# Performance work log

Hardware: AMD Instinct MI355X
Metric: run time of the kernel (lower is better)

The kernel has to match this reference:

```python
import jax, jax.numpy as jnp
import numpy as np


def _conv1x1(x, w, b):
    # x: [B, C, N], w: [O, C], b: [O]  (Conv1d with kernel_size=1)
    return jnp.einsum('bcn,oc->bon', x, w) + b[None, :, None]


def setup_inputs() -> dict:
    key = jax.random.key(0)
    ks = jax.random.split(key, 16)
    B, N, OD, A, H, M = 4096, 64, 128, 16, 64, 32
    s = jnp.float32(0.05)
    inp = {}
    inp['obs'] = jax.random.normal(ks[0], (B, OD, N), jnp.float32)
    inp['actions'] = jax.random.normal(ks[1], (N, B, A), jnp.float32)
    inp['relations'] = jax.random.uniform(ks[2], (N, B, N - 1), jnp.float32)
    # ObsEncode stand-in: 2-layer 1x1-conv MLP obs_dim -> 64 -> 64
    inp['enc_w1'] = jax.random.normal(ks[3], (H, OD), jnp.float32) * s
    inp['enc_b1'] = jnp.zeros((H,), jnp.float32)
    inp['enc_w2'] = jax.random.normal(ks[4], (H, H), jnp.float32) * s
    inp['enc_b2'] = jnp.zeros((H,), jnp.float32)
    C = H + A  # hidden_dim + act_dim = 80
    inp['cv_w1'] = jax.random.normal(ks[5], (M, C), jnp.float32) * s
    inp['cv_b1'] = jnp.zeros((M,), jnp.float32)
    inp['cv_w2'] = jax.random.normal(ks[6], (M // 2, M), jnp.float32) * s
    inp['cv_b2'] = jnp.zeros((M // 2,), jnp.float32)
    inp['sv_w1'] = jax.random.normal(ks[7], (M, C), jnp.float32) * s
    inp['sv_b1'] = jnp.zeros((M,), jnp.float32)
    inp['sv_w2'] = jax.random.normal(ks[8], (M // 2, M), jnp.float32) * s
    inp['sv_b2'] = jnp.zeros((M // 2,), jnp.float32)
    inp['pf_w'] = jax.random.normal(ks[9], (A, M), jnp.float32) * s
    inp['pf_b'] = jnp.zeros((A,), jnp.float32)
    inp['task'] = 0
    inp['agent_divide'] = N
    return inp


def reference(obs, actions, relations, enc_w1, enc_b1, enc_w2, enc_b2,
              cv_w1, cv_b1, cv_w2, cv_b2, sv_w1, sv_b1, sv_w2, sv_b2,
              pf_w, pf_b, task, agent_divide):
    N = relations.shape[0]
    # ObsEncode (use_relation=False): task/relations unused
    h = jax.nn.relu(_conv1x1(obs, enc_w1, enc_b1))
    h = _conv1x1(h, enc_w2, enc_b2)  # [B, 64, N]
    act = jnp.transpose(actions, (1, 2, 0))  # [B, A, N]
    sa = jnp.concatenate([h, act], axis=1)  # [B, 80, N]
    role1 = sa[:, :, :agent_divide]  # agent_divide == N -> full
    cv = _conv1x1(jax.nn.relu(_conv1x1(role1, cv_w1, cv_b1)), cv_w2, cv_b2)  # [B,16,N]
    sv = _conv1x1(jax.nn.relu(_conv1x1(role1, sv_w1, sv_b1)), sv_w2, sv_b2)  # [B,16,N]
    # build rel: insert self-weight 1 at column n_a for each agent (vectorized)
    n = jnp.arange(N)[:, None]  # agent index
    j = jnp.arange(N)[None, :]  # output column
    src = jnp.clip(jnp.where(j < n, j, j - 1), 0, N - 2)  # [N, N]
    g = jnp.take_along_axis(relations, src[:, None, :], axis=2)  # [N, B, N]
    rel = jnp.where((j == n)[:, None, :], jnp.float32(1.0), g)  # [N, B, N]
    rel = jnp.transpose(rel, (1, 2, 0))  # [B, N(cols j), N(agents)]
    cv = jnp.einsum('bcj,bjn->bcn', cv, rel)  # [B, 16, N]
    cat = jnp.concatenate([cv, sv], axis=1)  # [B, 32, N]
    post = _conv1x1(cat, pf_w, pf_b)  # [B, A, N]
    post = jnp.transpose(post, (2, 0, 1))  # [N, B, A]
    action_taken = jnp.argmax(actions, axis=2)[..., None]  # [N, B, 1]
    q = jnp.take_along_axis(post, action_taken, axis=2)  # [N, B, 1]
    return q
```

## Files before the change

kernel.cpp:

```cpp
#include <hip/hip_runtime.h>

namespace {
constexpr int Bb = 4096;
constexpr int Nn = 64;
constexpr int OD = 128;

constexpr int REL_OFF  = 0;
constexpr int CVV_OFF  = 4160;
constexpr int SVV_OFF  = 5184;
constexpr int PART_OFF = 6208;
}

typedef __attribute__((ext_vector_type(8))) _Float16 f16x8;
typedef __attribute__((ext_vector_type(4))) float    f32x4;

__device__ __forceinline__ void splitAs(const float* wrow, int k0, f16x8& ph, f16x8& pl) {
  float4 f0 = *(const float4*)(wrow + k0);
  float4 f1 = *(const float4*)(wrow + k0 + 4);
  float v[8] = {f0.x, f0.y, f0.z, f0.w, f1.x, f1.y, f1.z, f1.w};
#pragma unroll
  for (int i = 0; i < 8; ++i) {
    _Float16 h = (_Float16)v[i];
    ph[i] = h;
    pl[i] = (_Float16)((v[i] - (float)h) * 1024.f);
  }
}

__device__ __forceinline__ void loadBs(const float* X, int n, int k0,
                                       f16x8& bh, f16x8& bl) {
#pragma unroll
  for (int i = 0; i < 8; ++i) {
    float v = X[(k0 + i) * Nn + n];
    _Float16 h = (_Float16)v;
    bh[i] = h;
    bl[i] = (_Float16)((v - (float)h) * 1024.f);
  }
}

__global__ __launch_bounds__(256, 2)
void critic_fused(const float* __restrict__ obs,
                  const float* __restrict__ actions,
                  const float* __restrict__ relations,
                  const float* __restrict__ enc_w1, const float* __restrict__ enc_b1,
                  const float* __restrict__ enc_w2, const float* __restrict__ enc_b2,
                  const float* __restrict__ cv_w1, const float* __restrict__ cv_b1,
                  const float* __restrict__ cv_w2, const float* __restrict__ cv_b2,
                  const float* __restrict__ sv_w1, const float* __restrict__ sv_b1,
                  const float* __restrict__ sv_w2, const float* __restrict__ sv_b2,
                  const float* __restrict__ pf_w, const float* __restrict__ pf_b,
                  float* __restrict__ out)
{
  __shared__ float buf0[8192];
  __shared__ float buf1[4096];
  __shared__ float sa_s[96 * 64];
  __shared__ int   amax_s[64];

  const int tid = threadIdx.x;
  const int b = blockIdx.x;
  const int lane = tid & 63;
  const int w = tid >> 6;
  const int lo16 = lane & 15;
  const int hig  = lane >> 4;
  const int o0 = w * 16;

  {
    const float4* src = (const float4*)(obs + (size_t)b * OD * Nn);
    float4* dst = (float4*)buf0;
#pragma unroll
    for (int i = 0; i < 8; ++i) dst[tid + i * 256] = src[tid + i * 256];
  }
  for (int idx = tid; idx < Nn * 16; idx += 256) {
    int n = idx >> 4, a = idx & 15;
    sa_s[(64 + a) * Nn + n] = actions[((size_t)n * Bb + b) * 16 + a];
  }
  {
    float4* z = (float4*)(sa_s + 80 * Nn);
    z[tid] = make_float4(0.f, 0.f, 0.f, 0.f);
  }
  __syncthreads();

  {
    const float* wr = enc_w1 + (size_t)(o0 + lo16) * OD;
    f32x4 hac[4] = {};
    f32x4 lac[4] = {};
#pragma unroll
    for (int kk = 0; kk < 4; ++kk) {
      int k0 = kk * 32 + hig * 8;
      f16x8 ah, al;
      splitAs(wr, k0, ah, al);
#pragma unroll
      for (int t = 0; t < 4; ++t) {
        f16x8 bh, bl;
        loadBs(buf0, t * 16 + lo16, k0, bh, bl);
        hac[t] = __builtin_amdgcn_mfma_f32_16x16x32_f16(ah, bh, hac[t], 0, 0, 0);
        lac[t] = __builtin_amdgcn_mfma_f32_16x16x32_f16(ah, bl, lac[t], 0, 0, 0);
        lac[t] = __builtin_amdgcn_mfma_f32_16x16x32_f16(al, bh, lac[t], 0, 0, 0);
      }
    }
#pragma unroll
    for (int t = 0; t < 4; ++t)
#pragma unroll
      for (int r = 0; r < 4; ++r) {
        int o = o0 + hig * 4 + r;
        float v = hac[t][r] + lac[t][r] * (1.f / 1024.f) + enc_b1[o];
        buf1[o * Nn + t * 16 + lo16] = fmaxf(v, 0.f);
      }
  }
  __syncthreads();

  for (int idx = tid; idx < 4096; idx += 256) {
    int n = idx >> 6, k = idx & 63;
    if (k < 63) {
      float v = relations[((size_t)n * Bb + b) * 63 + k];
      int j = (k < n) ? k : k + 1;
      buf0[REL_OFF + n * 65 + j] = v;
    } else {
      buf0[REL_OFF + n * 65 + n] = 1.0f;
    }
  }
  if (tid < Nn) {
    float best = sa_s[64 * Nn + tid]; int bi = 0;
#pragma unroll
    for (int a = 1; a < 16; ++a) {
      float v = sa_s[(64 + a) * Nn + tid];
      if (v > best) { best = v; bi = a; }
    }
    amax_s[tid] = bi;
  }
  {
    const float* wr = enc_w2 + (size_t)(o0 + lo16) * 64;
    f32x4 hac[4] = {};
    f32x4 lac[4] = {};
#pragma unroll
    for (int kk = 0; kk < 2; ++kk) {
      int k0 = kk * 32 + hig * 8;
      f16x8 ah, al;
      splitAs(wr, k0, ah, al);
#pragma unroll
      for (int t = 0; t < 4; ++t) {
        f16x8 bh, bl;
        loadBs(buf1, t * 16 + lo16, k0, bh, bl);
        hac[t] = __builtin_amdgcn_mfma_f32_16x16x32_f16(ah, bh, hac[t], 0, 0, 0);
        lac[t] = __builtin_amdgcn_mfma_f32_16x16x32_f16(ah, bl, lac[t], 0, 0, 0);
        lac[t] = __builtin_amdgcn_mfma_f32_16x16x32_f16(al, bh, lac[t], 0, 0, 0);
      }
    }
#pragma unroll
    for (int t = 0; t < 4; ++t)
#pragma unroll
      for (int r = 0; r < 4; ++r) {
        int o = o0 + hig * 4 + r;
        sa_s[o * Nn + t * 16 + lo16] = hac[t][r] + lac[t][r] * (1.f / 1024.f) + enc_b2[o];
      }
  }
  __syncthreads();

  {
    int row = o0 + lo16;
    const float* wr = (row < 32) ? (cv_w1 + (size_t)row * 80)
                                 : (sv_w1 + (size_t)(row - 32) * 80);
    f32x4 hac[4] = {};
    f32x4 lac[4] = {};
#pragma unroll
    for (int kk = 0; kk < 3; ++kk) {
      int k0 = kk * 32 + hig * 8;
      f16x8 ah = {}, al = {};
      if (k0 < 80) splitAs(wr, k0, ah, al);
#pragma unroll
      for (int t = 0; t < 4; ++t) {
        f16x8 bh, bl;
        loadBs(sa_s, t * 16 + lo16, k0, bh, bl);
        hac[t] = __builtin_amdgcn_mfma_f32_16x16x32_f16(ah, bh, hac[t], 0, 0, 0);
        lac[t] = __builtin_amdgcn_mfma_f32_16x16x32_f16(ah, bl, lac[t], 0, 0, 0);
        lac[t] = __builtin_amdgcn_mfma_f32_16x16x32_f16(al, bh, lac[t], 0, 0, 0);
      }
    }
#pragma unroll
    for (int t = 0; t < 4; ++t)
#pragma unroll
      for (int r = 0; r < 4; ++r) {
        int o = o0 + hig * 4 + r;
        float bb = (o < 32) ? cv_b1[o] : sv_b1[o - 32];
        float v = hac[t][r] + lac[t][r] * (1.f / 1024.f) + bb;
        buf1[o * Nn + t * 16 + lo16] = fmaxf(v, 0.f);
      }
  }
  __syncthreads();

  {
    const int p4n0 = (tid & 31) * 2;
    const int p4o0 = (tid >> 5) * 4;
    const float* wr[4]; float bb[4];
    int srow; float* dst; int dro;
    if (p4o0 < 16) {
      srow = 0; dst = buf0 + CVV_OFF; dro = p4o0;
#pragma unroll
      for (int i = 0; i < 4; ++i) { wr[i] = cv_w2 + (p4o0 + i) * 32; bb[i] = cv_b2[p4o0 + i]; }
    } else {
      srow = 32; dst = buf0 + SVV_OFF; dro = p4o0 - 16;
#pragma unroll
      for (int i = 0; i < 4; ++i) { wr[i] = sv_w2 + (p4o0 + i - 16) * 32; bb[i] = sv_b2[p4o0 + i - 16]; }
    }
    float acc[4][2];
#pragma unroll
    for (int i = 0; i < 4; ++i) { acc[i][0] = bb[i]; acc[i][1] = bb[i]; }
#pragma unroll 2
    for (int c = 0; c < 32; c += 4) {
      float wv[4][4];
#pragma unroll
      for (int i = 0; i < 4; ++i) {
        float4 t = *(const float4*)(wr[i] + c);
        wv[i][0]=t.x; wv[i][1]=t.y; wv[i][2]=t.z; wv[i][3]=t.w;
      }
#pragma unroll
      for (int k = 0; k < 4; ++k) {
        float2 ov = *(const float2*)(buf1 + (srow + c + k) * Nn + p4n0);
#pragma unroll
        for (int i = 0; i < 4; ++i) {
          acc[i][0] = fmaf(wv[i][k], ov.x, acc[i][0]);
          acc[i][1] = fmaf(wv[i][k], ov.y, acc[i][1]);
        }
      }
    }
#pragma unroll
    for (int i = 0; i < 4; ++i)
      *(float2*)(dst + (dro + i) * Nn + p4n0) = make_float2(acc[i][0], acc[i][1]);
  }
  __syncthreads();

  {
    const int n = tid & 63, cg = tid >> 6;
    const float* cvv = buf0 + CVV_OFF;
    const float* svv = buf0 + SVV_OFF;
    const float* rel = buf0 + REL_OFF + n * 65;
    float acc[4] = {0.f, 0.f, 0.f, 0.f};
#pragma unroll 4
    for (int j = 0; j < 64; j += 4) {
      float r0 = rel[j], r1 = rel[j+1], r2 = rel[j+2], r3 = rel[j+3];
#pragma unroll
      for (int c4 = 0; c4 < 4; ++c4) {
        float4 cv = *(const float4*)(cvv + (cg * 4 + c4) * Nn + j);
        acc[c4] = fmaf(cv.x, r0, acc[c4]);
        acc[c4] = fmaf(cv.y, r1, acc[c4]);
        acc[c4] = fmaf(cv.z, r2, acc[c4]);
        acc[c4] = fmaf(cv.w, r3, acc[c4]);
      }
    }
    int a = amax_s[n];
    const float* pw = pf_w + a * 32;
    float part = 0.f;
#pragma unroll
    for (int c4 = 0; c4 < 4; ++c4) {
      part = fmaf(acc[c4], pw[cg * 4 + c4], part);
      part = fmaf(svv[(cg * 4 + c4) * Nn + n], pw[16 + cg * 4 + c4], part);
    }
    buf0[PART_OFF + cg * 64 + n] = part;
  }
  __syncthreads();

  if (tid < Nn) {
    float q = pf_b[amax_s[tid]]
            + buf0[PART_OFF + tid]       + buf0[PART_OFF + 64 + tid]
            + buf0[PART_OFF + 128 + tid] + buf0[PART_OFF + 192 + tid];
    out[(size_t)tid * Bb + b] = q;
  }
}

extern "C" void kernel_launch(void* const* d_in, const int* in_sizes, int n_in,
                              void* d_out, int out_size, void* d_ws, size_t ws_size,
                              hipStream_t stream) {
  const float* obs       = (const float*)d_in[0];
  const float* actions   = (const float*)d_in[1];
  const float* relations = (const float*)d_in[2];
  const float* enc_w1    = (const float*)d_in[3];
  const float* enc_b1    = (const float*)d_in[4];
  const float* enc_w2    = (const float*)d_in[5];
  const float* enc_b2    = (const float*)d_in[6];
  const float* cv_w1     = (const float*)d_in[7];
  const float* cv_b1     = (const float*)d_in[8];
  const float* cv_w2     = (const float*)d_in[9];
  const float* cv_b2     = (const float*)d_in[10];
  const float* sv_w1     = (const float*)d_in[11];
  const float* sv_b1     = (const float*)d_in[12];
  const float* sv_w2     = (const float*)d_in[13];
  const float* sv_b2     = (const float*)d_in[14];
  const float* pf_w      = (const float*)d_in[15];
  const float* pf_b      = (const float*)d_in[16];

  critic_fused<<<dim3(Bb), dim3(256), 0, stream>>>(
      obs, actions, relations,
      enc_w1, enc_b1, enc_w2, enc_b2,
      cv_w1, cv_b1, cv_w2, cv_b2,
      sv_w1, sv_b1, sv_w2, sv_b2,
      pf_w, pf_b, (float*)d_out);
}
```

Measured before the change: 159.0 us.

## Pre-split weights into fp16 fragments and stage swizzled fp16 activations in LDS

A small pre-kernel converts the MFMA weights once per call into hi/lo fp16 pairs laid out in per-lane fragment order in the workspace. The main kernel then loads each weight fragment with one vector load instead of splitting it per block. Activations are converted to hi/lo fp16 once when written to shared memory, using an XOR-swizzled n-major layout, so B operands are read as 16-byte vectors instead of eight strided scalar reads with repeated conversion. It adds an extra kernel launch and a workspace dependency, and reorganises shared memory, which changes LDS usage and may affect occupancy.

```diff
diff --git a/kernel.cpp b/kernel.cpp
--- a/kernel.cpp
+++ b/kernel.cpp
@@ -5,55 +5,87 @@
 constexpr int Nn = 64;
 constexpr int OD = 128;
 
-constexpr int REL_OFF  = 0;
-constexpr int CVV_OFF  = 4160;
-constexpr int SVV_OFF  = 5184;
-constexpr int PART_OFF = 6208;
+constexpr int E1H = 0;
+constexpr int E1L = 8192;
+constexpr int E2H = 16384;
+constexpr int E2L = 20480;
+constexpr int C1H = 24576;
+constexpr int C1L = 30720;
+constexpr int WS_ELEMS = 36864;
 }
 
 typedef __attribute__((ext_vector_type(8))) _Float16 f16x8;
+typedef __attribute__((ext_vector_type(4))) _Float16 f16x4;
 typedef __attribute__((ext_vector_type(4))) float    f32x4;
 
-__device__ __forceinline__ void splitAs(const float* wrow, int k0, f16x8& ph, f16x8& pl) {
-  float4 f0 = *(const float4*)(wrow + k0);
-  float4 f1 = *(const float4*)(wrow + k0 + 4);
-  float v[8] = {f0.x, f0.y, f0.z, f0.w, f1.x, f1.y, f1.z, f1.w};
-#pragma unroll
-  for (int i = 0; i < 8; ++i) {
-    _Float16 h = (_Float16)v[i];
-    ph[i] = h;
-    pl[i] = (_Float16)((v[i] - (float)h) * 1024.f);
-  }
-}
-
-__device__ __forceinline__ void loadBs(const float* X, int n, int k0,
-                                       f16x8& bh, f16x8& bl) {
-#pragma unroll
-  for (int i = 0; i < 8; ++i) {
-    float v = X[(k0 + i) * Nn + n];
-    _Float16 h = (_Float16)v;
-    bh[i] = h;
-    bl[i] = (_Float16)((v - (float)h) * 1024.f);
-  }
+__device__ __forceinline__ int swz(int n, int rowb, int k) {
+  return n * rowb + ((2 * k) ^ ((n & 7) << 4));
+}
+__device__ __forceinline__ int swz4(int n, int rowb, int k) {
+  return n * rowb + ((2 * k) ^ ((n & 3) << 4));
+}
+
+__global__ __launch_bounds__(256)
+void prep_weights(const float* __restrict__ ew1, const float* __restrict__ ew2,
+                  const float* __restrict__ cw1, const float* __restrict__ sw1,
+                  _Float16* __restrict__ ws) {
+  int idx = blockIdx.x * 256 + threadIdx.x;
+  if (idx >= 18432) return;
+  int pos, hbase, lbase;
+  float v;
+  if (idx < 8192) {
+    pos = idx; hbase = E1H; lbase = E1L;
+    int frag = pos >> 9, r = pos & 511, lane = r >> 3, i = r & 7;
+    int w = frag >> 2, kk = frag & 3;
+    int row = w * 16 + (lane & 15), k = kk * 32 + (lane >> 4) * 8 + i;
+    v = ew1[row * 128 + k];
+  } else if (idx < 12288) {
+    pos = idx - 8192; hbase = E2H; lbase = E2L;
+    int frag = pos >> 9, r = pos & 511, lane = r >> 3, i = r & 7;
+    int w = frag >> 1, kk = frag & 1;
+    int row = w * 16 + (lane & 15), k = kk * 32 + (lane >> 4) * 8 + i;
+    v = ew2[row * 64 + k];
+  } else {
+    pos = idx - 12288; hbase = C1H; lbase = C1L;
+    int frag = pos >> 9, r = pos & 511, lane = r >> 3, i = r & 7;
+    int w = frag / 3, kk = frag % 3;
+    int row = w * 16 + (lane & 15), k = kk * 32 + (lane >> 4) * 8 + i;
+    v = 0.f;
+    if (k < 80) v = (row < 32) ? cw1[row * 80 + k] : sw1[(row - 32) * 80 + k];
+  }
+  _Float16 h = (_Float16)v;
+  ws[hbase + pos] = h;
+  ws[lbase + pos] = (_Float16)((v - (float)h) * 1024.f);
 }
 
 __global__ __launch_bounds__(256, 2)
 void critic_fused(const float* __restrict__ obs,
                   const float* __restrict__ actions,
                   const float* __restrict__ relations,
-                  const float* __restrict__ enc_w1, const float* __restrict__ enc_b1,
-                  const float* __restrict__ enc_w2, const float* __restrict__ enc_b2,
-                  const float* __restrict__ cv_w1, const float* __restrict__ cv_b1,
+                  const float* __restrict__ enc_b1, const float* __restrict__ enc_b2,
+                  const float* __restrict__ cv_b1,  const float* __restrict__ sv_b1,
                   const float* __restrict__ cv_w2, const float* __restrict__ cv_b2,
-                  const float* __restrict__ sv_w1, const float* __restrict__ sv_b1,
                   const float* __restrict__ sv_w2, const float* __restrict__ sv_b2,
                   const float* __restrict__ pf_w, const float* __restrict__ pf_b,
+                  const _Float16* __restrict__ ws,
                   float* __restrict__ out)
 {
-  __shared__ float buf0[8192];
-  __shared__ float buf1[4096];
-  __shared__ float sa_s[96 * 64];
-  __shared__ int   amax_s[64];
+  __shared__ float rel_s[64 * 65];
+  __shared__ __align__(16) char RA[32768];
+  __shared__ __align__(16) char RB[16384];
+  __shared__ __align__(16) char RC[8192];
+  __shared__ int amax_s[64];
+
+  char* X0h = RA;
+  char* X0l = RA + 16384;
+  char* sah = RA;
+  char* sal = RA + 8192;
+  float* X3 = (float*)(RA + 16384);
+  char* X1h = RB;
+  char* X1l = RB + 8192;
+  float* csv  = (float*)RB;
+  char* acth = RC;
+  char* actl = RC + 4096;
 
   const int tid = threadIdx.x;
   const int b = blockIdx.x;
@@ -62,49 +94,81 @@
   const int lo16 = lane & 15;
   const int hig  = lane >> 4;
   const int o0 = w * 16;
-
-  {
-    const float4* src = (const float4*)(obs + (size_t)b * OD * Nn);
-    float4* dst = (float4*)buf0;
-#pragma unroll
-    for (int i = 0; i < 8; ++i) dst[tid + i * 256] = src[tid + i * 256];
-  }
-  for (int idx = tid; idx < Nn * 16; idx += 256) {
-    int n = idx >> 4, a = idx & 15;
-    sa_s[(64 + a) * Nn + n] = actions[((size_t)n * Bb + b) * 16 + a];
-  }
-  {
-    float4* z = (float4*)(sa_s + 80 * Nn);
-    z[tid] = make_float4(0.f, 0.f, 0.f, 0.f);
-  }
-  __syncthreads();
-
-  {
-    const float* wr = enc_w1 + (size_t)(o0 + lo16) * OD;
-    f32x4 hac[4] = {};
-    f32x4 lac[4] = {};
+  const f16x8* wsv = (const f16x8*)ws;
+
+  {
+    int n = tid & 63, chunk = tid >> 6;
+    const float* p = obs + (size_t)b * (OD * Nn) + (size_t)chunk * 32 * Nn + n;
+#pragma unroll
+    for (int g = 0; g < 4; ++g) {
+      f16x8 uh, ul;
+#pragma unroll
+      for (int j = 0; j < 8; ++j) {
+        float v = p[(g * 8 + j) * Nn];
+        _Float16 h = (_Float16)v;
+        uh[j] = h;
+        ul[j] = (_Float16)((v - (float)h) * 1024.f);
+      }
+      int off = swz(n, 256, chunk * 32 + g * 8);
+      *(f16x8*)(X0h + off) = uh;
+      *(f16x8*)(X0l + off) = ul;
+    }
+  }
+  {
+    int n = tid >> 2, a0 = (tid & 3) * 4;
+    float4 v4 = *(const float4*)(actions + ((size_t)n * Bb + b) * 16 + a0);
+    float vv[4] = {v4.x, v4.y, v4.z, v4.w};
+    f16x4 uh, ul;
+#pragma unroll
+    for (int r = 0; r < 4; ++r) {
+      _Float16 h = (_Float16)vv[r];
+      uh[r] = h;
+      ul[r] = (_Float16)((vv[r] - (float)h) * 1024.f);
+    }
+    int offa = swz4(n, 64, a0);
+    *(f16x4*)(acth + offa) = uh;
+    *(f16x4*)(actl + offa) = ul;
+    f16x4 z = {};
+    int offz = swz4(n, 64, 16 + a0);
+    *(f16x4*)(acth + offz) = z;
+    *(f16x4*)(actl + offz) = z;
+  }
+  __syncthreads();
+
+  {
+    f32x4 hac[4] = {}, lac[4] = {};
 #pragma unroll
     for (int kk = 0; kk < 4; ++kk) {
+      int frag = w * 4 + kk;
+      f16x8 ah = wsv[(E1H >> 3) + frag * 64 + lane];
+      f16x8 al = wsv[(E1L >> 3) + frag * 64 + lane];
       int k0 = kk * 32 + hig * 8;
-      f16x8 ah, al;
-      splitAs(wr, k0, ah, al);
 #pragma unroll
       for (int t = 0; t < 4; ++t) {
-        f16x8 bh, bl;
-        loadBs(buf0, t * 16 + lo16, k0, bh, bl);
+        int off = swz(t * 16 + lo16, 256, k0);
+        f16x8 bh = *(const f16x8*)(X0h + off);
+        f16x8 bl = *(const f16x8*)(X0l + off);
         hac[t] = __builtin_amdgcn_mfma_f32_16x16x32_f16(ah, bh, hac[t], 0, 0, 0);
         lac[t] = __builtin_amdgcn_mfma_f32_16x16x32_f16(ah, bl, lac[t], 0, 0, 0);
         lac[t] = __builtin_amdgcn_mfma_f32_16x16x32_f16(al, bh, lac[t], 0, 0, 0);
       }
     }
 #pragma unroll
-    for (int t = 0; t < 4; ++t)
+    for (int t = 0; t < 4; ++t) {
+      f16x4 ph, pl;
 #pragma unroll
       for (int r = 0; r < 4; ++r) {
         int o = o0 + hig * 4 + r;
         float v = hac[t][r] + lac[t][r] * (1.f / 1024.f) + enc_b1[o];
-        buf1[o * Nn + t * 16 + lo16] = fmaxf(v, 0.f);
-      }
+        v = fmaxf(v, 0.f);
+        _Float16 h = (_Float16)v;
+        ph[r] = h;
+        pl[r] = (_Float16)((v - (float)h) * 1024.f);
+      }
+      int off = swz(t * 16 + lo16, 128, o0 + hig * 4);
+      *(f16x4*)(X1h + off) = ph;
+      *(f16x4*)(X1l + off) = pl;
+    }
   }
   __syncthreads();
 
@@ -113,63 +177,77 @@
     if (k < 63) {
       float v = relations[((size_t)n * Bb + b) * 63 + k];
       int j = (k < n) ? k : k + 1;
-      buf0[REL_OFF + n * 65 + j] = v;
+      rel_s[n * 65 + j] = v;
     } else {
-      buf0[REL_OFF + n * 65 + n] = 1.0f;
+      rel_s[n * 65 + n] = 1.0f;
     }
   }
   if (tid < Nn) {
-    float best = sa_s[64 * Nn + tid]; int bi = 0;
+    const float* ar = actions + ((size_t)tid * Bb + b) * 16;
+    float best = ar[0]; int bi = 0;
 #pragma unroll
     for (int a = 1; a < 16; ++a) {
-      float v = sa_s[(64 + a) * Nn + tid];
+      float v = ar[a];
       if (v > best) { best = v; bi = a; }
     }
     amax_s[tid] = bi;
   }
   {
-    const float* wr = enc_w2 + (size_t)(o0 + lo16) * 64;
-    f32x4 hac[4] = {};
-    f32x4 lac[4] = {};
+    f32x4 hac[4] = {}, lac[4] = {};
 #pragma unroll
     for (int kk = 0; kk < 2; ++kk) {
+      int frag = w * 2 + kk;
+      f16x8 ah = wsv[(E2H >> 3) + frag * 64 + lane];
+      f16x8 al = wsv[(E2L >> 3) + frag * 64 + lane];
       int k0 = kk * 32 + hig * 8;
-      f16x8 ah, al;
-      splitAs(wr, k0, ah, al);
 #pragma unroll
       for (int t = 0; t < 4; ++t) {
-        f16x8 bh, bl;
-        loadBs(buf1, t * 16 + lo16, k0, bh, bl);
+        int off = swz(t * 16 + lo16, 128, k0);
+        f16x8 bh = *(const f16x8*)(X1h + off);
+        f16x8 bl = *(const f16x8*)(X1l + off);
         hac[t] = __builtin_amdgcn_mfma_f32_16x16x32_f16(ah, bh, hac[t], 0, 0, 0);
         lac[t] = __builtin_amdgcn_mfma_f32_16x16x32_f16(ah, bl, lac[t], 0, 0, 0);
         lac[t] = __builtin_amdgcn_mfma_f32_16x16x32_f16(al, bh, lac[t], 0, 0, 0);
       }
     }
 #pragma unroll
-    for (int t = 0; t < 4; ++t)
+    for (int t = 0; t < 4; ++t) {
+      f16x4 ph, pl;
 #pragma unroll
       for (int r = 0; r < 4; ++r) {
         int o = o0 + hig * 4 + r;
-        sa_s[o * Nn + t * 16 + lo16] = hac[t][r] + lac[t][r] * (1.f / 1024.f) + enc_b2[o];
-      }
-  }
-  __syncthreads();
-
-  {
-    int row = o0 + lo16;
-    const float* wr = (row < 32) ? (cv_w1 + (size_t)row * 80)
-                                 : (sv_w1 + (size_t)(row - 32) * 80);
-    f32x4 hac[4] = {};
-    f32x4 lac[4] = {};
+        float v = hac[t][r] + lac[t][r] * (1.f / 1024.f) + enc_b2[o];
+        _Float16 h = (_Float16)v;
+        ph[r] = h;
+        pl[r] = (_Float16)((v - (float)h) * 1024.f);
+      }
+      int off = swz(t * 16 + lo16, 128, o0 + hig * 4);
+      *(f16x4*)(sah + off) = ph;
+      *(f16x4*)(sal + off) = pl;
+    }
+  }
+  __syncthreads();
+
+  {
+    f32x4 hac[4] = {}, lac[4] = {};
 #pragma unroll
     for (int kk = 0; kk < 3; ++kk) {
-      int k0 = kk * 32 + hig * 8;
-      f16x8 ah = {}, al = {};
-      if (k0 < 80) splitAs(wr, k0, ah, al);
+      int frag = w * 3 + kk;
+      f16x8 ah = wsv[(C1H >> 3) + frag * 64 + lane];
+      f16x8 al = wsv[(C1L >> 3) + frag * 64 + lane];
 #pragma unroll
       for (int t = 0; t < 4; ++t) {
+        int n = t * 16 + lo16;
         f16x8 bh, bl;
-        loadBs(sa_s, t * 16 + lo16, k0, bh, bl);
+        if (kk < 2) {
+          int off = swz(n, 128, kk * 32 + hig * 8);
+          bh = *(const f16x8*)(sah + off);
+          bl = *(const f16x8*)(sal + off);
+        } else {
+          int off = swz4(n, 64, hig * 8);
+          bh = *(const f16x8*)(acth + off);
+          bl = *(const f16x8*)(actl + off);
+        }
         hac[t] = __builtin_amdgcn_mfma_f32_16x16x32_f16(ah, bh, hac[t], 0, 0, 0);
         lac[t] = __builtin_amdgcn_mfma_f32_16x16x32_f16(ah, bl, lac[t], 0, 0, 0);
         lac[t] = __builtin_amdgcn_mfma_f32_16x16x32_f16(al, bh, lac[t], 0, 0, 0);
@@ -182,7 +260,7 @@
         int o = o0 + hig * 4 + r;
         float bb = (o < 32) ? cv_b1[o] : sv_b1[o - 32];
         float v = hac[t][r] + lac[t][r] * (1.f / 1024.f) + bb;
-        buf1[o * Nn + t * 16 + lo16] = fmaxf(v, 0.f);
+        X3[o * Nn + t * 16 + lo16] = fmaxf(v, 0.f);
       }
   }
   __syncthreads();
@@ -193,11 +271,11 @@
     const float* wr[4]; float bb[4];
     int srow; float* dst; int dro;
     if (p4o0 < 16) {
-      srow = 0; dst = buf0 + CVV_OFF; dro = p4o0;
+      srow = 0; dst = csv; dro = p4o0;
 #pragma unroll
       for (int i = 0; i < 4; ++i) { wr[i] = cv_w2 + (p4o0 + i) * 32; bb[i] = cv_b2[p4o0 + i]; }
     } else {
-      srow = 32; dst = buf0 + SVV_OFF; dro = p4o0 - 16;
+      srow = 32; dst = csv + 1024; dro = p4o0 - 16;
 #pragma unroll
       for (int i = 0; i < 4; ++i) { wr[i] = sv_w2 + (p4o0 + i - 16) * 32; bb[i] = sv_b2[p4o0 + i - 16]; }
     }
@@ -214,7 +292,7 @@
       }
 #pragma unroll
       for (int k = 0; k < 4; ++k) {
-        float2 ov = *(const float2*)(buf1 + (srow + c + k) * Nn + p4n0);
+        float2 ov = *(const float2*)(X3 + (srow + c + k) * Nn + p4n0);
 #pragma unroll
         for (int i = 0; i < 4; ++i) {
           acc[i][0] = fmaf(wv[i][k], ov.x, acc[i][0]);
@@ -230,13 +308,13 @@
 
   {
     const int n = tid & 63, cg = tid >> 6;
-    const float* cvv = buf0 + CVV_OFF;
-    const float* svv = buf0 + SVV_OFF;
-    const float* rel = buf0 + REL_OFF + n * 65;
+    const float* cvv = csv;
+    const float* svv = csv + 1024;
+    const float* relr = rel_s + n * 65;
     float acc[4] = {0.f, 0.f, 0.f, 0.f};
 #pragma unroll 4
     for (int j = 0; j < 64; j += 4) {
-      float r0 = rel[j], r1 = rel[j+1], r2 = rel[j+2], r3 = rel[j+3];
+      float r0 = relr[j], r1 = relr[j+1], r2 = relr[j+2], r3 = relr[j+3];
 #pragma unroll
       for (int c4 = 0; c4 < 4; ++c4) {
         float4 cv = *(const float4*)(cvv + (cg * 4 + c4) * Nn + j);
@@ -254,14 +332,14 @@
       part = fmaf(acc[c4], pw[cg * 4 + c4], part);
       part = fmaf(svv[(cg * 4 + c4) * Nn + n], pw[16 + cg * 4 + c4], part);
     }
-    buf0[PART_OFF + cg * 64 + n] = part;
+    csv[2048 + cg * 64 + n] = part;
   }
   __syncthreads();
 
   if (tid < Nn) {
     float q = pf_b[amax_s[tid]]
-            + buf0[PART_OFF + tid]       + buf0[PART_OFF + 64 + tid]
-            + buf0[PART_OFF + 128 + tid] + buf0[PART_OFF + 192 + tid];
+            + csv[2048 + tid]       + csv[2048 + 64 + tid]
+            + csv[2048 + 128 + tid] + csv[2048 + 192 + tid];
     out[(size_t)tid * Bb + b] = q;
   }
 }
@@ -287,10 +365,14 @@
   const float* pf_w      = (const float*)d_in[15];
   const float* pf_b      = (const float*)d_in[16];
 
+  _Float16* ws = (_Float16*)d_ws;
+
+  prep_weights<<<dim3((18432 + 255) / 256), dim3(256), 0, stream>>>(
+      enc_w1, enc_w2, cv_w1, sv_w1, ws);
+
   critic_fused<<<dim3(Bb), dim3(256), 0, stream>>>(
       obs, actions, relations,
-      enc_w1, enc_b1, enc_w2, enc_b2,
-      cv_w1, cv_b1, cv_w2, cv_b2,
-      sv_w1, sv_b1, sv_w2, sv_b2,
-      pf_w, pf_b, (float*)d_out);
-}
+      enc_b1, enc_b2, cv_b1, sv_b1,
+      cv_w2, cv_b2, sv_w2, sv_b2,
+      pf_w, pf_b, ws, (float*)d_out);
+}
```

Result: faster. 132.7 us (-16.6%).
